# Kernel optimization log

Hardware: AMD Instinct MI355X
Metric: run time of the kernel (lower is better)

## Reference

```python
import jax, jax.numpy as jnp
import numpy as np

EPS = 1e-12  # F.normalize default eps


def _unfold(x, k, pad, stride):
    # torch F.unfold: [B,C,H,W] -> [B, C*k*k, L], features ordered (c, kh, kw), L row-major.
    B, C, H, W = x.shape
    xp = jnp.pad(x, ((0, 0), (0, 0), (pad, pad), (pad, pad)))
    Ho = (H + 2 * pad - k) // stride + 1
    Wo = (W + 2 * pad - k) // stride + 1
    r = (jnp.arange(Ho) * stride)[:, None] + jnp.arange(k)[None, :]  # [Ho,k]
    c = (jnp.arange(Wo) * stride)[:, None] + jnp.arange(k)[None, :]  # [Wo,k]
    p = xp[:, :, r[:, None, :, None], c[None, :, None, :]]  # [B,C,Ho,Wo,k,k]
    return p.transpose(0, 1, 4, 5, 2, 3).reshape(B, C * k * k, Ho * Wo)


def _fold(p, out_hw, k, pad, stride):
    # torch F.fold: overlap-add inverse of _unfold.
    B, CKK, L = p.shape
    C = CKK // (k * k)
    H, W = out_hw
    Ho = (H + 2 * pad - k) // stride + 1
    Wo = (W + 2 * pad - k) // stride + 1
    p = p.reshape(B, C, k, k, Ho, Wo).transpose(0, 1, 4, 5, 2, 3)  # [B,C,Ho,Wo,k,k]
    r = (jnp.arange(Ho) * stride)[:, None] + jnp.arange(k)[None, :]
    c = (jnp.arange(Wo) * stride)[:, None] + jnp.arange(k)[None, :]
    out = jnp.zeros((B, C, H + 2 * pad, W + 2 * pad), p.dtype)
    out = out.at[:, :, r[:, None, :, None], c[None, :, None, :]].add(p)
    return out[:, :, pad:pad + H, pad:pad + W]


def _l2n(x, axis):
    n = jnp.sqrt(jnp.sum(x * x, axis=axis, keepdims=True))
    return x / jnp.maximum(n, EPS)


def setup_inputs() -> dict:
    key = jax.random.key(0)
    ks = jax.random.split(key, 11)
    B, H, W = 1, 32, 32
    f = jnp.float32
    return {
        'lrsr_lv3': jax.random.normal(ks[0], (B, 256, H, W), f),
        'refsr_lv1': jax.random.normal(ks[1], (B, 64, 4 * H, 4 * W), f),
        'refsr_lv2': jax.random.normal(ks[2], (B, 128, 2 * H, 2 * W), f),
        'refsr_lv3': jax.random.normal(ks[3], (B, 256, H, W), f),
        'ref_lv1': jax.random.normal(ks[4], (B, 64, 4 * H, 4 * W), f),
        'ref_lv2': jax.random.normal(ks[5], (B, 128, 2 * H, 2 * W), f),
        'ref_lv3': jax.random.normal(ks[6], (B, 256, H, W), f),
        'W1': jax.random.normal(ks[7], (2304, 1152), f) * 0.02,
        'b1': jax.random.normal(ks[8], (2304,), f) * 0.02,
        'W2': jax.random.normal(ks[9], (2304, 576), f) * 0.02,
        'b2': jax.random.normal(ks[10], (2304,), f) * 0.02,
    }


def reference(lrsr_lv3, refsr_lv1, refsr_lv2, refsr_lv3, ref_lv1, ref_lv2, ref_lv3, W1, b1, W2, b2):
    B, _, H, W = lrsr_lv3.shape
    lr3 = _unfold(lrsr_lv3, 3, 1, 1)                       # [B, 2304, N]
    r3 = _unfold(refsr_lv3, 3, 1, 1).transpose(0, 2, 1)    # [B, N3, 2304]
    r2 = _unfold(refsr_lv2, 3, 1, 1).transpose(0, 2, 1) @ W1.T + b1  # [B, N2, 2304]
    r1 = _unfold(refsr_lv1, 3, 1, 1).transpose(0, 2, 1) @ W2.T + b2  # [B, N1, 2304]
    r3 = _l2n(r3, 2); r2 = _l2n(r2, 2); r1 = _l2n(r1, 2)
    lr3 = _l2n(lr3, 1)
    R3 = jnp.einsum('bnd,bdm->bnm', r3, lr3)  # [B, N3, N]
    R2 = jnp.einsum('bnd,bdm->bnm', r2, lr3)  # [B, N2, N]
    R1 = jnp.einsum('bnd,bdm->bnm', r1, lr3)  # [B, N1, N]
    R3_star = jnp.max(R3, axis=1); R3_arg = jnp.argmax(R3, axis=1)
    R2_star = jnp.max(R2, axis=1)
    R1_star = jnp.max(R1, axis=1)
    ref3u = _unfold(ref_lv3, 3, 1, 1)
    ref2u = _unfold(ref_lv2, 6, 2, 2)
    ref1u = _unfold(ref_lv1, 12, 4, 4)
    idx = R3_arg[:, None, :]  # [B,1,N] broadcast over feature dim
    T3u = jnp.take_along_axis(ref3u, idx, axis=2)
    T2u = jnp.take_along_axis(ref2u, idx, axis=2)
    T1u = jnp.take_along_axis(ref1u, idx, axis=2)
    T_lv3 = _fold(T3u, (H, W), 3, 1, 1) / 9.0
    T_lv2 = _fold(T2u, (2 * H, 2 * W), 6, 2, 2) / 9.0
    T_lv1 = _fold(T1u, (4 * H, 4 * W), 12, 4, 4) / 9.0
    S_3 = R3_star.reshape(B, 1, H, W)
    S_2 = R2_star.reshape(B, 1, H, W)
    S_1 = R1_star.reshape(B, 1, H, W)
    return (S_1, S_2, S_3, T_lv3, T_lv2, T_lv1)
```

## Files before the change

### kernel.cpp

```cpp
#include <hip/hip_runtime.h>

typedef short bf8 __attribute__((ext_vector_type(8)));
typedef float f32x4 __attribute__((ext_vector_type(4)));

static __device__ __forceinline__ unsigned short f2bf(float f) {
  unsigned u = __float_as_uint(f);
  unsigned r = u + 0x7FFFu + ((u >> 16) & 1u);
  return (unsigned short)(r >> 16);
}
static __device__ __forceinline__ float bf2f(unsigned short h) {
  return __uint_as_float(((unsigned)h) << 16);
}
static __device__ __forceinline__ unsigned fkey(float f) {
  unsigned u = __float_as_uint(f);
  return (u & 0x80000000u) ? ~u : (u | 0x80000000u);
}
static __device__ __forceinline__ float kdec(unsigned k) {
  unsigned u = (k & 0x80000000u) ? (k & 0x7FFFFFFFu) : ~k;
  return __uint_as_float(u);
}
static __device__ __forceinline__ int permC(int c, int C) { return (c % 9) * C + c / 9; }

static __device__ __forceinline__ void gload_lds16(const unsigned short* g, unsigned short* l) {
  __builtin_amdgcn_global_load_lds((const __attribute__((address_space(1))) void*)g,
                                   (__attribute__((address_space(3))) void*)l, 16, 0, 0);
}

static __device__ __forceinline__ float uf3(const float* __restrict__ src, int lgS, int d, int m) {
  const int S = 1 << lgS;
  int cc = d / 9;
  int r9 = d - cc * 9;
  int ki = r9 / 3;
  int kj = r9 - ki * 3;
  int i = (m >> lgS) + ki - 1;
  int j = (m & (S - 1)) + kj - 1;
  if ((unsigned)i >= (unsigned)S || (unsigned)j >= (unsigned)S) return 0.f;
  return src[((size_t)cc << (2 * lgS)) + ((size_t)i << lgS) + j];
}

__global__ __launch_bounds__(256) void k_prepA(const float* __restrict__ lrsr3, const float* __restrict__ rsr3,
                                               const float* __restrict__ rsr2, const float* __restrict__ rsr1,
                                               const float* __restrict__ b1, const float* __restrict__ b2,
                                               float* __restrict__ sclr, float* __restrict__ scu3,
                                               float* __restrict__ bl2, float* __restrict__ bl1,
                                               float* __restrict__ G2,
                                               float* __restrict__ rsr2t, float* __restrict__ rsr1t) {
  __shared__ float Tt[64][65];
  const int blk = blockIdx.x;
  const int tid = threadIdx.x;
  if (blk < 2048) {
    __shared__ float r0[256], r1[256], r2[256];
    const bool lr = blk < 1024;
    const int m = blk & 1023;
    const float* src = lr ? lrsr3 : rsr3;
    float s = 0.f, d1 = 0.f, d2 = 0.f;
    for (int d = tid; d < 2304; d += 256) {
      float v = uf3(src, 5, d, m);
      s += v * v; d1 += b1[d] * v; d2 += b2[d] * v;
    }
    r0[tid] = s; r1[tid] = d1; r2[tid] = d2;
    __syncthreads();
    for (int o = 128; o > 0; o >>= 1) {
      if (tid < o) { r0[tid] += r0[tid + o]; r1[tid] += r1[tid + o]; r2[tid] += r2[tid + o]; }
      __syncthreads();
    }
    if (tid == 0) {
      float sc = 1.f / fmaxf(sqrtf(r0[0]), 1e-12f);
      if (lr) { sclr[m] = sc; bl2[m] = r1[0] * sc; bl1[m] = r2[0] * sc; }
      else    { scu3[m] = sc; }
    }
  } else if (blk < 3072) {
    __shared__ float As[16][32], Bs[16][32];
    const int px = blk - 2048;
    const int m0 = (px >> 5) * 32, n0 = (px & 31) * 32;
    const int tx = tid & 15, ty = tid >> 4;
    float acc[2][2] = {};
    for (int kb = 0; kb < 256; kb += 16) {
      __syncthreads();
      {
        int kk = tid >> 5, mm = tid & 31;
        As[kk][mm] = lrsr3[(size_t)(kb + kk) * 1024 + m0 + mm];
        Bs[kk][mm] = rsr3[(size_t)(kb + kk) * 1024 + n0 + mm];
        int e2 = tid + 256; int kk2 = e2 >> 5, mm2 = e2 & 31;
        As[kk2][mm2] = lrsr3[(size_t)(kb + kk2) * 1024 + m0 + mm2];
        Bs[kk2][mm2] = rsr3[(size_t)(kb + kk2) * 1024 + n0 + mm2];
      }
      __syncthreads();
#pragma unroll
      for (int kk = 0; kk < 16; ++kk) {
        float a0 = As[kk][ty * 2], a1 = As[kk][ty * 2 + 1];
        float b0 = Bs[kk][tx * 2], b1v = Bs[kk][tx * 2 + 1];
        acc[0][0] = fmaf(a0, b0, acc[0][0]); acc[0][1] = fmaf(a0, b1v, acc[0][1]);
        acc[1][0] = fmaf(a1, b0, acc[1][0]); acc[1][1] = fmaf(a1, b1v, acc[1][1]);
      }
    }
#pragma unroll
    for (int i = 0; i < 2; ++i)
#pragma unroll
      for (int jj = 0; jj < 2; ++jj)
        G2[(size_t)(m0 + ty * 2 + i) * 1024 + (n0 + tx * 2 + jj)] = acc[i][jj];
  } else if (blk < 3200) {
    const int idx = blk - 3072;
    const int ct = idx & 1, st = idx >> 1;
#pragma unroll
    for (int i = 0; i < 16; ++i) {
      int id = tid + i * 256;
      int r = id >> 6, c = id & 63;
      Tt[r][c] = rsr2[(size_t)(ct * 64 + r) * 4096 + st * 64 + c];
    }
    __syncthreads();
#pragma unroll
    for (int i = 0; i < 16; ++i) {
      int id = tid + i * 256;
      int cc2 = id >> 6, rr = id & 63;
      rsr2t[(size_t)(st * 64 + cc2) * 128 + ct * 64 + rr] = Tt[rr][cc2];
    }
  } else {
    const int st = blk - 3200;
#pragma unroll
    for (int i = 0; i < 16; ++i) {
      int id = tid + i * 256;
      int r = id >> 6, c = id & 63;
      Tt[r][c] = rsr1[(size_t)r * 16384 + st * 64 + c];
    }
    __syncthreads();
#pragma unroll
    for (int i = 0; i < 16; ++i) {
      int id = tid + i * 256;
      int cc2 = id >> 6, rr = id & 63;
      rsr1t[(size_t)(st * 64 + cc2) * 64 + rr] = Tt[rr][cc2];
    }
  }
}

__global__ __launch_bounds__(256) void k_prepB(const float* __restrict__ lrsr3,
                                               const float* __restrict__ rsr2t, const float* __restrict__ rsr1t,
                                               const float* __restrict__ W1, const float* __restrict__ W2,
                                               const float* __restrict__ b1, const float* __restrict__ b2,
                                               const float* __restrict__ sclr, const float* __restrict__ scu3,
                                               const float* __restrict__ G2,
                                               unsigned short* __restrict__ lr3nbT,
                                               unsigned short* __restrict__ U2b, unsigned short* __restrict__ U1b,
                                               unsigned short* __restrict__ W1t, unsigned short* __restrict__ W2t,
                                               float* __restrict__ bw2, float* __restrict__ bw1,
                                               float* __restrict__ bb,
                                               float* __restrict__ s3, int* __restrict__ arg) {
  __shared__ unsigned short Ls[64][65];
  __shared__ float bv[256]; __shared__ int bidx[256];
  const int blk = blockIdx.x;
  const int tid = threadIdx.x;
  if (blk < 1152) {
    int id8 = blk * 256 + tid;
    int m = id8 / 288, c0 = (id8 - m * 288) * 8;
    float sc = sclr[m];
    bf8 v;
#pragma unroll
    for (int e = 0; e < 8; ++e) v[e] = (short)f2bf(uf3(lrsr3, 5, c0 + e, m) * sc);
    *(bf8*)(lr3nbT + (size_t)m * 2304 + c0) = v;
  } else if (blk < 3456) {
    int id = (blk - 1152) * 256 + tid;
    int t = id & 15, rest = id >> 4;
    int kk = rest % 9, n = rest / 9;
    int cc0 = t * 8;
    int ki = kk / 3, kj = kk - ki * 3;
    int sy = (n >> 6) + ki - 1, sx = (n & 63) + kj - 1;
    bf8 v;
    if ((unsigned)sy < 64u && (unsigned)sx < 64u) {
      const float* p = rsr2t + (size_t)(sy * 64 + sx) * 128 + cc0;
      f32x4 a = *(const f32x4*)p;
      f32x4 bq = *(const f32x4*)(p + 4);
#pragma unroll
      for (int e = 0; e < 4; ++e) { v[e] = (short)f2bf(a[e]); v[4 + e] = (short)f2bf(bq[e]); }
    } else {
#pragma unroll
      for (int e = 0; e < 8; ++e) v[e] = 0;
    }
    *(bf8*)(U2b + (size_t)n * 1152 + kk * 128 + cc0) = v;
  } else if (blk < 8576) {
    int id = (blk - 3456) * 256 + tid;
    int n = id / 80, rem = id - n * 80;
    int ks = rem >> 3, t = rem & 7;
    int cc0 = t * 8;
    bf8 v;
    if (ks == 9) {
#pragma unroll
      for (int e = 0; e < 8; ++e) v[e] = 0;
    } else {
      int ki = ks / 3, kj = ks - ki * 3;
      int sy = (n >> 7) + ki - 1, sx = (n & 127) + kj - 1;
      if ((unsigned)sy < 128u && (unsigned)sx < 128u) {
        const float* p = rsr1t + (size_t)(sy * 128 + sx) * 64 + cc0;
        f32x4 a = *(const f32x4*)p;
        f32x4 bq = *(const f32x4*)(p + 4);
#pragma unroll
        for (int e = 0; e < 4; ++e) { v[e] = (short)f2bf(a[e]); v[4 + e] = (short)f2bf(bq[e]); }
      } else {
#pragma unroll
        for (int e = 0; e < 8; ++e) v[e] = 0;
      }
    }
    *(bf8*)(U1b + (size_t)n * 640 + ks * 64 + cc0) = v;
  } else if (blk < 9548) {
    int idx = blk - 8576;
    int xx = idx % 27, yy = idx / 27;
    const float* W; unsigned short* Wt; int Cw, c0;
    if (xx < 18) { W = W1; Wt = W1t; Cw = 1152; c0 = xx * 64; }
    else         { W = W2; Wt = W2t; Cw = 576;  c0 = (xx - 18) * 64; }
    const int Cch = Cw / 9;
    const int d0 = yy * 64;
#pragma unroll
    for (int i = 0; i < 16; ++i) {
      int id = tid + i * 256;
      int r = id >> 6, c = id & 63;
      Ls[r][c] = f2bf(W[(size_t)(d0 + r) * Cw + c0 + c]);
    }
    __syncthreads();
#pragma unroll
    for (int i = 0; i < 16; ++i) {
      int id = tid + i * 256;
      int cc = id >> 6, rr = id & 63;
      int c = c0 + cc;
      Wt[(size_t)((c % 9) * Cch + c / 9) * 2304 + d0 + rr] = Ls[rr][cc];
    }
  } else if (blk < 9628) {
    int idx = blk - 9548;
    int x = idx & 7, y = idx >> 3;
    if (y == 9) {
      if (x >= 2) return;
      const float* b = x ? b2 : b1;
      float s = 0.f;
      for (int d = tid; d < 2304; d += 256) s += b[d] * b[d];
      bv[tid] = s; __syncthreads();
      for (int o = 128; o > 0; o >>= 1) { if (tid < o) bv[tid] += bv[tid + o]; __syncthreads(); }
      if (tid == 0) bb[x] = bv[0];
      return;
    }
    const bool two = x < 5;
    const float* W = two ? W1 : W2;
    const float* b = two ? b1 : b2;
    float* bw = two ? bw2 : bw1;
    const int Cw = two ? 1152 : 576;
    int c = (two ? x : x - 5) * 256 + tid;
    if (c >= Cw) return;
    int d0 = y * 256;
    float s = 0.f;
    for (int d = d0; d < d0 + 256; ++d) s += b[d] * W[(size_t)d * Cw + c];
    atomicAdd(&bw[(c % 9) * (Cw / 9) + c / 9], s);
  } else {
    const int m = blk - 9628;
    const int mi = m >> 5, mj = m & 31;
    float best = -3.0e38f; int bi = 0;
    for (int n = tid; n < 1024; n += 256) {
      const int ni = n >> 5, nj = n & 31;
      float raw = 0.f;
#pragma unroll
      for (int dy = -1; dy <= 1; ++dy) {
#pragma unroll
        for (int dx = -1; dx <= 1; ++dx) {
          bool vm = ((unsigned)(mi + dy) < 32u) && ((unsigned)(mj + dx) < 32u);
          bool vn = ((unsigned)(ni + dy) < 32u) && ((unsigned)(nj + dx) < 32u);
          if (vm && vn) {
            int off = dy * 32 + dx;
            raw += G2[(size_t)(m + off) * 1024 + (n + off)];
          }
        }
      }
      float v = raw * scu3[n];
      if (v > best) { best = v; bi = n; }
    }
    bv[tid] = best; bidx[tid] = bi;
    __syncthreads();
    for (int o = 128; o > 0; o >>= 1) {
      if (tid < o) {
        float ov = bv[tid + o]; int oi = bidx[tid + o];
        if (ov > bv[tid] || (ov == bv[tid] && oi < bidx[tid])) { bv[tid] = ov; bidx[tid] = oi; }
      }
      __syncthreads();
    }
    if (tid == 0) { s3[m] = bv[0] * sclr[m]; arg[m] = bidx[0]; }
  }
}

struct Job {
  const unsigned short* Alo;
  const unsigned short* Ahi;
  const unsigned short* Bt;
  unsigned short* Clo;
  unsigned short* Chi;
  const float* bl;
  const float* bw;
  const float* bbp;
  float* pnsq;
  float* pbwd;
  float* cmax;
  int Msplit, N, K, nbx, Mtot, npart, which;
};

template <int EPI, int NBUF>
static __device__ __forceinline__ void gemm_body(const Job& j0, const Job& j1, int nb0) {
  __shared__ __align__(16) unsigned short As[NBUF][128 * 64];
  __shared__ __align__(16) unsigned short Bs[NBUF][128 * 64];
  __shared__ unsigned colkey[128];
  __shared__ float ninvL[128];

  const int nwg = (int)gridDim.x;
  const int h = (int)blockIdx.x;
  const int qq = nwg >> 3, rm = nwg & 7;
  const int xcd = h & 7, wth = h >> 3;
  const int bid = (xcd < rm ? xcd * (qq + 1) : rm * (qq + 1) + (xcd - rm) * qq) + wth;

  const bool first = (bid < nb0);
  const Job j = first ? j0 : j1;
  const int local = bid - (first ? 0 : nb0);
  const int by = local / j.nbx;
  const int bx = local - by * j.nbx;
  const int m0 = by * 128, n0 = bx * 128;
  const int K = j.K, N = j.N;

  const unsigned short* Abase = (m0 < j.Msplit)
      ? j.Alo + (size_t)m0 * K
      : j.Ahi + (size_t)(m0 - j.Msplit) * K;

  const int tid = threadIdx.x;
  const int l = tid & 63;
  const int w = tid >> 6;
  const int wr = w >> 1, wc = w & 1;
  if (EPI == 2) {
    if (tid < 128) {
      colkey[tid] = 0u;
      const int r = m0 + tid;
      float nsq = 0.f, bwd = 0.f;
      for (int p = 0; p < j.npart; ++p) {
        nsq += j.pnsq[(size_t)p * j.Mtot + r];
        bwd += j.pbwd[(size_t)p * j.Mtot + r];
      }
      float tq = nsq + 2.f * bwd + j.bbp[j.which];
      ninvL[tid] = 1.f / fmaxf(sqrtf(fmaxf(tq, 0.f)), 1e-12f);
    }
  }

  f32x4 acc[4][4] = {};

  const int srow = w * 32;
  const int lrow = l >> 3;
  const int gcol = ((l & 7) ^ lrow) * 8;
  const int mr = l & 15;
  const int kg = l >> 4;

  const int nt = K >> 6;
  const int snap_kb = n0 + wc * 64;
  unsigned short snap[4][4][4];

  auto stage = [&](int buf, int kb) {
#pragma unroll
    for (int i = 0; i < 4; ++i) {
      int r = srow + i * 8;
      gload_lds16(Abase + (size_t)(r + lrow) * K + kb + gcol, &As[buf][r * 64]);
      gload_lds16(j.Bt + (size_t)(n0 + r + lrow) * K + kb + gcol, &Bs[buf][r * 64]);
    }
  };
  auto compute_tile = [&](int cur) {
#pragma unroll
    for (int ks = 0; ks < 2; ++ks) {
      bf8 af[4], bv[4];
#pragma unroll
      for (int mi = 0; mi < 4; ++mi) {
        const int row = wr * 64 + mi * 16 + mr;
        af[mi] = *(const bf8*)&As[cur][row * 64 + (((ks * 4 + kg) ^ (row & 7)) * 8)];
      }
#pragma unroll
      for (int ni = 0; ni < 4; ++ni) {
        const int row = wc * 64 + ni * 16 + mr;
        bv[ni] = *(const bf8*)&Bs[cur][row * 64 + (((ks * 4 + kg) ^ (row & 7)) * 8)];
      }
      __builtin_amdgcn_s_setprio(1);
#pragma unroll
      for (int mi = 0; mi < 4; ++mi)
#pragma unroll
        for (int ni = 0; ni < 4; ++ni)
          acc[mi][ni] = __builtin_amdgcn_mfma_f32_16x16x32_bf16(af[mi], bv[ni], acc[mi][ni], 0, 0, 0);
      __builtin_amdgcn_s_setprio(0);
    }
  };
  auto do_snap = [&](int cur) {
#pragma unroll
    for (int mi = 0; mi < 4; ++mi)
#pragma unroll
      for (int e = 0; e < 4; ++e) {
        const int row = wr * 64 + mi * 16 + kg * 4 + e;
#pragma unroll
        for (int ni = 0; ni < 4; ++ni) {
          const int slot = ni * 2 + (mr >> 3);
          snap[mi][ni][e] = As[cur][row * 64 + ((slot ^ (row & 7)) * 8) + (mr & 7)];
        }
      }
  };

  if constexpr (NBUF == 1) {
    for (int t = 0; t < nt; ++t) {
      if (t) __syncthreads();
      stage(0, t << 6);
      __syncthreads();
      compute_tile(0);
      if (EPI == 1 && (t << 6) == snap_kb) do_snap(0);
    }
  } else {
    auto waitv = [&](int Wt) {
      if (Wt >= 2)      asm volatile("s_waitcnt vmcnt(16)\ns_barrier" ::: "memory");
      else if (Wt == 1) asm volatile("s_waitcnt vmcnt(8)\ns_barrier" ::: "memory");
      else              asm volatile("s_waitcnt vmcnt(0)\ns_barrier" ::: "memory");
    };
#pragma unroll
    for (int p = 0; p < NBUF; ++p) if (p < nt) stage(p, p << 6);
    { int inflight = (NBUF < nt ? NBUF : nt); waitv(inflight - 1); }
    int cur = 0;
    for (int t = 0; t < nt; ++t) {
      compute_tile(cur);
      if (EPI == 1 && (t << 6) == snap_kb) do_snap(cur);
      if (t + 1 < nt) {
        asm volatile("s_waitcnt lgkmcnt(0)\ns_barrier" ::: "memory");
        if (t + NBUF < nt) stage(cur, (t + NBUF) << 6);
        const int im = (nt - 1 < t + NBUF) ? (nt - 1) : (t + NBUF);
        waitv(im - (t + 1));
        cur = (cur + 1 == NBUF) ? 0 : cur + 1;
      }
    }
  }

  const int lr0 = wr * 64;
  const int lc0 = wc * 64;
  if (EPI == 0) {
    unsigned short* Cbase = (m0 < j.Msplit)
        ? j.Clo + (size_t)m0 * N
        : j.Chi + (size_t)(m0 - j.Msplit) * N;
#pragma unroll
    for (int mi = 0; mi < 4; ++mi)
#pragma unroll
      for (int ni = 0; ni < 4; ++ni)
#pragma unroll
        for (int e = 0; e < 4; ++e)
          Cbase[(size_t)(lr0 + mi * 16 + kg * 4 + e) * (size_t)N + (n0 + lc0 + ni * 16 + mr)] = f2bf(acc[mi][ni][e]);
  } else if (EPI == 1) {
    float rp[4][4] = {};
    float bp[4][4] = {};
#pragma unroll
    for (int ni = 0; ni < 4; ++ni) {
      const float bwv = j.bw[n0 + lc0 + ni * 16 + mr];
#pragma unroll
      for (int mi = 0; mi < 4; ++mi)
#pragma unroll
        for (int e = 0; e < 4; ++e) {
          const float av = bf2f(snap[mi][ni][e]);
          rp[mi][e] += acc[mi][ni][e] * av;
          bp[mi][e] += bwv * av;
        }
    }
#pragma unroll
    for (int off = 1; off < 16; off <<= 1)
#pragma unroll
      for (int mi = 0; mi < 4; ++mi)
#pragma unroll
        for (int e = 0; e < 4; ++e) {
          rp[mi][e] += __shfl_xor(rp[mi][e], off);
          bp[mi][e] += __shfl_xor(bp[mi][e], off);
        }
    if (mr == 0) {
      const size_t slotbase = (size_t)(bx * 2 + wc) * j.Mtot;
#pragma unroll
      for (int mi = 0; mi < 4; ++mi)
#pragma unroll
        for (int e = 0; e < 4; ++e) {
          const int r = m0 + lr0 + mi * 16 + kg * 4 + e;
          j.pnsq[slotbase + r] = rp[mi][e];
          j.pbwd[slotbase + r] = bp[mi][e];
        }
    }
  } else {
    float nv[4][4];
#pragma unroll
    for (int mi = 0; mi < 4; ++mi)
#pragma unroll
      for (int e = 0; e < 4; ++e)
        nv[mi][e] = ninvL[lr0 + mi * 16 + kg * 4 + e];
#pragma unroll
    for (int ni = 0; ni < 4; ++ni) {
      float blv = j.bl[n0 + lc0 + ni * 16 + mr];
      float mx = -3.0e38f;
#pragma unroll
      for (int mi = 0; mi < 4; ++mi)
#pragma unroll
        for (int e = 0; e < 4; ++e) mx = fmaxf(mx, (acc[mi][ni][e] + blv) * nv[mi][e]);
      atomicMax(&colkey[lc0 + ni * 16 + mr], fkey(mx));
    }
    __syncthreads();
    if (tid < 128) j.cmax[(size_t)by * 1024 + n0 + tid] = kdec(colkey[tid]);
  }
}

__global__ __launch_bounds__(256) void k_gP (Job a, Job b, int nb0) { gemm_body<0, 3>(a, b, nb0); }
__global__ __launch_bounds__(256) void k_gE1(Job a, Job b, int nb0) { gemm_body<1, 1>(a, b, nb0); }
__global__ __launch_bounds__(256) void k_gE2(Job a, Job b, int nb0) { gemm_body<2, 1>(a, b, nb0); }

__global__ __launch_bounds__(256) void k_tfold(const float* __restrict__ ref3, const float* __restrict__ ref2,
                                               const float* __restrict__ ref1, const int* __restrict__ arg,
                                               const float* __restrict__ cmax1, const float* __restrict__ cmax2,
                                               float* __restrict__ out) {
  const int bid = blockIdx.x;
  const int tid = threadIdx.x;
  if (bid < 256) {
    __shared__ float plane[1024];
    __shared__ int argL[1024];
    const int c = bid;
#pragma unroll
    for (int k = 0; k < 4; ++k) {
      plane[k * 256 + tid] = ref3[(size_t)c * 1024 + k * 256 + tid];
      argL[k * 256 + tid] = arg[k * 256 + tid];
    }
    __syncthreads();
#pragma unroll
    for (int k = 0; k < 4; ++k) {
      int px = k * 256 + tid;
      int y = px >> 5, x = px & 31;
      float s = 0.f;
#pragma unroll
      for (int di = -1; di <= 1; ++di) {
        int i = y + di;
        if ((unsigned)i >= 32u) continue;
#pragma unroll
        for (int dj = -1; dj <= 1; ++dj) {
          int jw = x + dj;
          if ((unsigned)jw >= 32u) continue;
          int n2 = argL[i * 32 + jw];
          int rr = (n2 >> 5) + y - i, cc = (n2 & 31) + x - jw;
          if ((unsigned)rr < 32u && (unsigned)cc < 32u) s += plane[rr * 32 + cc];
        }
      }
      out[3072 + (size_t)c * 1024 + px] = s * (1.f / 9.f);
    }
  } else if (bid < 1280) {
    __shared__ int argL[1024];
#pragma unroll
    for (int k = 0; k < 4; ++k) argL[k * 256 + tid] = arg[k * 256 + tid];
    __syncthreads();
    int id2 = (bid - 256) * 256 + tid;
    int q = id2 & 31, y = (id2 >> 5) & 63, c = id2 >> 11;
    int iy = y >> 1;
    float s0 = 0.f, s1 = 0.f;
#pragma unroll
    for (int di = -1; di <= 1; ++di) {
      int i = iy + di;
      if ((unsigned)i >= 32u) continue;
      int ry = y - 2 * i;
#pragma unroll
      for (int dj = -1; dj <= 1; ++dj) {
        int jw = q + dj;
        if ((unsigned)jw >= 32u) continue;
        int n2 = argL[i * 32 + jw];
        int rr = (n2 >> 5) * 2 + ry;
        int cb = (n2 & 31) * 2 + 2 * (q - jw);
        if ((unsigned)rr < 64u && (unsigned)cb < 63u) {
          const float* p = ref2 + (size_t)c * 4096 + rr * 64 + cb;
          s0 += p[0]; s1 += p[1];
        }
      }
    }
    float2 o; o.x = s0 * (1.f / 9.f); o.y = s1 * (1.f / 9.f);
    *(float2*)(out + 265216 + (size_t)c * 4096 + y * 64 + 2 * q) = o;
  } else if (bid < 2304) {
    __shared__ int argL[1024];
#pragma unroll
    for (int k = 0; k < 4; ++k) argL[k * 256 + tid] = arg[k * 256 + tid];
    __syncthreads();
    int id1 = (bid - 1280) * 256 + tid;
    int q = id1 & 31, y = (id1 >> 5) & 127, c = id1 >> 12;
    int iy = y >> 2;
    f32x4 s = {0.f, 0.f, 0.f, 0.f};
#pragma unroll
    for (int di = -1; di <= 1; ++di) {
      int i = iy + di;
      if ((unsigned)i >= 32u) continue;
      int ry = y - 4 * i;
#pragma unroll
      for (int dj = -1; dj <= 1; ++dj) {
        int jw = q + dj;
        if ((unsigned)jw >= 32u) continue;
        int n2 = argL[i * 32 + jw];
        int rr = (n2 >> 5) * 4 + ry;
        int cb = (n2 & 31) * 4 + 4 * (q - jw);
        if ((unsigned)rr < 128u && (unsigned)cb < 125u) {
          f32x4 v = *(const f32x4*)(ref1 + (size_t)c * 16384 + rr * 128 + cb);
          s += v;
        }
      }
    }
    s *= (1.f / 9.f);
    *(f32x4*)(out + 789504 + (size_t)c * 16384 + y * 128 + 4 * q) = s;
  } else {
    int t = (bid - 2304) * 256 + tid;
    if (t < 1024) {
      float mx = -3.0e38f;
      for (int rb = 0; rb < 128; ++rb) mx = fmaxf(mx, cmax1[rb * 1024 + t]);
      out[t] = mx;
    } else {
      int tt = t - 1024;
      float mx = -3.0e38f;
      for (int rb = 0; rb < 32; ++rb) mx = fmaxf(mx, cmax2[rb * 1024 + tt]);
      out[1024 + tt] = mx;
    }
  }
}

static constexpr size_t OFF_BW2     = 0;
static constexpr size_t OFF_BW1     = 4608;
static constexpr size_t ZERO_BYTES  = 7168;
static constexpr size_t OFF_BB      = 7168;
static constexpr size_t OFF_BL2     = 7424;
static constexpr size_t OFF_BL1     = 11520;
static constexpr size_t OFF_SCLR    = 15616;
static constexpr size_t OFF_SCU3    = 19712;
static constexpr size_t OFF_R3ARG   = 23808;
static constexpr size_t OFF_PNSQ2   = 27904;
static constexpr size_t OFF_PBWD2   = OFF_PNSQ2 + 294912;
static constexpr size_t OFF_PNSQ1   = OFF_PBWD2 + 294912;
static constexpr size_t OFF_PBWD1   = OFF_PNSQ1 + 655360;
static constexpr size_t OFF_CMAX2   = OFF_PBWD1 + 655360;
static constexpr size_t OFF_CMAX1   = OFF_CMAX2 + 131072;
static constexpr size_t OFF_LR3NBT  = OFF_CMAX1 + 524288;
static constexpr size_t OFF_U2B     = OFF_LR3NBT + 4718592;
static constexpr size_t OFF_U1B     = OFF_U2B    + 9437184;
static constexpr size_t OFF_W1T     = OFF_U1B    + 20971520;
static constexpr size_t OFF_W2T     = OFF_W1T    + 5308416;
static constexpr size_t OFF_A2      = OFF_W2T    + 2949120;
static constexpr size_t OFF_A1      = OFF_A2     + 2654208;
static constexpr size_t OFF_M2T     = OFF_A1     + 819200;
static constexpr size_t OFF_M1T     = OFF_M2T    + 2359296;
static constexpr size_t OFF_G2      = OFF_M1T    + 1310720;
static constexpr size_t OFF_R2T     = OFF_G2     + 4194304;
static constexpr size_t OFF_R1T     = OFF_R2T    + 2097152;

extern "C" void kernel_launch(void* const* d_in, const int* in_sizes, int n_in,
                              void* d_out, int out_size, void* d_ws, size_t ws_size,
                              hipStream_t stream) {
  (void)in_sizes; (void)n_in; (void)out_size; (void)ws_size;
  const float* lrsr3  = (const float*)d_in[0];
  const float* rsr1   = (const float*)d_in[1];
  const float* rsr2   = (const float*)d_in[2];
  const float* rsr3   = (const float*)d_in[3];
  const float* ref1   = (const float*)d_in[4];
  const float* ref2   = (const float*)d_in[5];
  const float* ref3   = (const float*)d_in[6];
  const float* W1     = (const float*)d_in[7];
  const float* b1     = (const float*)d_in[8];
  const float* W2     = (const float*)d_in[9];
  const float* b2     = (const float*)d_in[10];
  float* out = (float*)d_out;
  char* ws = (char*)d_ws;

  float*          bw2     = (float*)(ws + OFF_BW2);
  float*          bw1     = (float*)(ws + OFF_BW1);
  float*          bb      = (float*)(ws + OFF_BB);
  float*          bl2     = (float*)(ws + OFF_BL2);
  float*          bl1     = (float*)(ws + OFF_BL1);
  float*          sclr    = (float*)(ws + OFF_SCLR);
  float*          scu3    = (float*)(ws + OFF_SCU3);
  int*            R3arg   = (int*)(ws + OFF_R3ARG);
  float*          pnsq2   = (float*)(ws + OFF_PNSQ2);
  float*          pbwd2   = (float*)(ws + OFF_PBWD2);
  float*          pnsq1   = (float*)(ws + OFF_PNSQ1);
  float*          pbwd1   = (float*)(ws + OFF_PBWD1);
  float*          cmax2   = (float*)(ws + OFF_CMAX2);
  float*          cmax1   = (float*)(ws + OFF_CMAX1);
  unsigned short* lr3nbT  = (unsigned short*)(ws + OFF_LR3NBT);
  unsigned short* U2b     = (unsigned short*)(ws + OFF_U2B);
  unsigned short* U1b     = (unsigned short*)(ws + OFF_U1B);
  unsigned short* W1t     = (unsigned short*)(ws + OFF_W1T);
  unsigned short* W2t     = (unsigned short*)(ws + OFF_W2T);
  unsigned short* A2b     = (unsigned short*)(ws + OFF_A2);
  unsigned short* A1b     = (unsigned short*)(ws + OFF_A1);
  unsigned short* M2tb    = (unsigned short*)(ws + OFF_M2T);
  unsigned short* M1tb    = (unsigned short*)(ws + OFF_M1T);
  float*          G2      = (float*)(ws + OFF_G2);
  float*          rsr2t   = (float*)(ws + OFF_R2T);
  float*          rsr1t   = (float*)(ws + OFF_R1T);

  hipMemsetAsync(d_ws, 0, ZERO_BYTES, stream);
  hipMemsetAsync(ws + OFF_W2T + (size_t)576 * 2304 * 2, 0, (size_t)64 * 2304 * 2, stream);

  k_prepA<<<3456, 256, 0, stream>>>(lrsr3, rsr3, rsr2, rsr1, b1, b2, sclr, scu3, bl2, bl1, G2, rsr2t, rsr1t);
  k_prepB<<<10652, 256, 0, stream>>>(lrsr3, rsr2t, rsr1t, W1, W2, b1, b2, sclr, scu3, G2,
                                     lr3nbT, U2b, U1b, W1t, W2t, bw2, bw1, bb, out + 2048, R3arg);

  Job jz = {};

  {
    Job a = jz, b = jz;
    a.Alo = W1t; a.Ahi = lr3nbT; a.Msplit = 1152; a.Bt = W1t;
    a.Clo = A2b; a.Chi = M2tb; a.N = 1152; a.K = 2304; a.nbx = 9;
    b.Alo = W2t; b.Ahi = lr3nbT; b.Msplit = 640; b.Bt = W2t;
    b.Clo = A1b; b.Chi = M1tb; b.N = 640; b.K = 2304; b.nbx = 5;
    k_gP<<<153 + 65, 256, 0, stream>>>(a, b, 153);
  }
  {
    Job a = jz, b = jz;
    a.Alo = U2b; a.Ahi = U2b; a.Msplit = 4096; a.Bt = A2b;
    a.bw = bw2; a.pnsq = pnsq2; a.pbwd = pbwd2; a.Mtot = 4096;
    a.N = 1152; a.K = 1152; a.nbx = 9;
    b.Alo = U1b; b.Ahi = U1b; b.Msplit = 16384; b.Bt = A1b;
    b.bw = bw1; b.pnsq = pnsq1; b.pbwd = pbwd1; b.Mtot = 16384;
    b.N = 640; b.K = 640; b.nbx = 5;
    k_gE1<<<288 + 640, 256, 0, stream>>>(a, b, 288);
  }
  {
    Job a = jz, b = jz;
    a.Alo = U2b; a.Ahi = U2b; a.Msplit = 4096; a.Bt = M2tb;
    a.bl = bl2; a.pnsq = pnsq2; a.pbwd = pbwd2; a.bbp = bb;
    a.npart = 18; a.which = 0; a.cmax = cmax2; a.Mtot = 4096;
    a.N = 1024; a.K = 1152; a.nbx = 8;
    b.Alo = U1b; b.Ahi = U1b; b.Msplit = 16384; b.Bt = M1tb;
    b.bl = bl1; b.pnsq = pnsq1; b.pbwd = pbwd1; b.bbp = bb;
    b.npart = 10; b.which = 1; b.cmax = cmax1; b.Mtot = 16384;
    b.N = 1024; b.K = 640; b.nbx = 8;
    k_gE2<<<256 + 1024, 256, 0, stream>>>(a, b, 256);
  }

  k_tfold<<<2312, 256, 0, stream>>>(ref3, ref2, ref1, R3arg, cmax1, cmax2, out);
}
```

Measured before the change: 256.5 us.

## Fuse weight transpose and projection GEMM into prep kernels, apply row scale in epilogue

Moves the lr3 unfold-to-bf16 and the W1/W2 transpose into the first prep kernel. The projection GEMM (k_gP) now runs as the first 218 blocks of a merged kernel alongside the remaining prep work (U2b/U1b packing, bias dots, R3 argmax). The lr3 row normalization scale is dropped from the packed operand and applied in the GEMM epilogue instead. This saves one kernel launch and lets the GEMM overlap with independent prep blocks. In exchange the GEMM switches from triple-buffered to single-buffered staging and shares a launch with many small memory-bound blocks.

```diff
diff --git a/kernel.cpp b/kernel.cpp
--- a/kernel.cpp
+++ b/kernel.cpp
@@ -19,7 +19,11 @@
   unsigned u = (k & 0x80000000u) ? (k & 0x7FFFFFFFu) : ~k;
   return __uint_as_float(u);
 }
-static __device__ __forceinline__ int permC(int c, int C) { return (c % 9) * C + c / 9; }
+static __device__ __forceinline__ int xcdswz(int h, int nwg) {
+  int q = nwg >> 3, r = nwg & 7;
+  int xcd = h & 7, w = h >> 3;
+  return (xcd < r ? xcd * (q + 1) : r * (q + 1) + (xcd - r) * q) + w;
+}
 
 static __device__ __forceinline__ void gload_lds16(const unsigned short* g, unsigned short* l) {
   __builtin_amdgcn_global_load_lds((const __attribute__((address_space(1))) void*)g,
@@ -40,12 +44,14 @@
 
 __global__ __launch_bounds__(256) void k_prepA(const float* __restrict__ lrsr3, const float* __restrict__ rsr3,
                                                const float* __restrict__ rsr2, const float* __restrict__ rsr1,
+                                               const float* __restrict__ W1, const float* __restrict__ W2,
                                                const float* __restrict__ b1, const float* __restrict__ b2,
                                                float* __restrict__ sclr, float* __restrict__ scu3,
                                                float* __restrict__ bl2, float* __restrict__ bl1,
                                                float* __restrict__ G2,
-                                               float* __restrict__ rsr2t, float* __restrict__ rsr1t) {
-  __shared__ float Tt[64][65];
+                                               float* __restrict__ rsr2t, float* __restrict__ rsr1t,
+                                               unsigned short* __restrict__ lr3nbT,
+                                               unsigned short* __restrict__ W1t, unsigned short* __restrict__ W2t) {
   const int blk = blockIdx.x;
   const int tid = threadIdx.x;
   if (blk < 2048) {
@@ -100,6 +106,7 @@
       for (int jj = 0; jj < 2; ++jj)
         G2[(size_t)(m0 + ty * 2 + i) * 1024 + (n0 + tx * 2 + jj)] = acc[i][jj];
   } else if (blk < 3200) {
+    __shared__ float Tt[64][65];
     const int idx = blk - 3072;
     const int ct = idx & 1, st = idx >> 1;
 #pragma unroll
@@ -115,7 +122,8 @@
       int cc2 = id >> 6, rr = id & 63;
       rsr2t[(size_t)(st * 64 + cc2) * 128 + ct * 64 + rr] = Tt[rr][cc2];
     }
-  } else {
+  } else if (blk < 3456) {
+    __shared__ float Tt[64][65];
     const int st = blk - 3200;
 #pragma unroll
     for (int i = 0; i < 16; ++i) {
@@ -130,35 +138,273 @@
       int cc2 = id >> 6, rr = id & 63;
       rsr1t[(size_t)(st * 64 + cc2) * 64 + rr] = Tt[rr][cc2];
     }
-  }
-}
-
-__global__ __launch_bounds__(256) void k_prepB(const float* __restrict__ lrsr3,
-                                               const float* __restrict__ rsr2t, const float* __restrict__ rsr1t,
-                                               const float* __restrict__ W1, const float* __restrict__ W2,
-                                               const float* __restrict__ b1, const float* __restrict__ b2,
-                                               const float* __restrict__ sclr, const float* __restrict__ scu3,
-                                               const float* __restrict__ G2,
-                                               unsigned short* __restrict__ lr3nbT,
-                                               unsigned short* __restrict__ U2b, unsigned short* __restrict__ U1b,
-                                               unsigned short* __restrict__ W1t, unsigned short* __restrict__ W2t,
-                                               float* __restrict__ bw2, float* __restrict__ bw1,
-                                               float* __restrict__ bb,
-                                               float* __restrict__ s3, int* __restrict__ arg) {
-  __shared__ unsigned short Ls[64][65];
-  __shared__ float bv[256]; __shared__ int bidx[256];
+  } else if (blk < 4608) {
+    int id8 = (blk - 3456) * 256 + tid;
+    int m = id8 / 288, c0 = (id8 - m * 288) * 8;
+    bf8 v;
+#pragma unroll
+    for (int e = 0; e < 8; ++e) v[e] = (short)f2bf(uf3(lrsr3, 5, c0 + e, m));
+    *(bf8*)(lr3nbT + (size_t)m * 2304 + c0) = v;
+  } else {
+    __shared__ unsigned short Ls[64][65];
+    int idx = blk - 4608;
+    int xx = idx % 27, yy = idx / 27;
+    const float* W; unsigned short* Wt; int Cw, c0;
+    if (xx < 18) { W = W1; Wt = W1t; Cw = 1152; c0 = xx * 64; }
+    else         { W = W2; Wt = W2t; Cw = 576;  c0 = (xx - 18) * 64; }
+    const int Cch = Cw / 9;
+    const int d0 = yy * 64;
+#pragma unroll
+    for (int i = 0; i < 16; ++i) {
+      int id = tid + i * 256;
+      int r = id >> 6, c = id & 63;
+      Ls[r][c] = f2bf(W[(size_t)(d0 + r) * Cw + c0 + c]);
+    }
+    __syncthreads();
+#pragma unroll
+    for (int i = 0; i < 16; ++i) {
+      int id = tid + i * 256;
+      int cc = id >> 6, rr = id & 63;
+      int c = c0 + cc;
+      Wt[(size_t)((c % 9) * Cch + c / 9) * 2304 + d0 + rr] = Ls[rr][cc];
+    }
+  }
+}
+
+struct Job {
+  const unsigned short* Alo;
+  const unsigned short* Ahi;
+  const unsigned short* Bt;
+  unsigned short* Clo;
+  unsigned short* Chi;
+  const float* bl;
+  const float* bw;
+  const float* bbp;
+  const float* rowscale;
+  float* pnsq;
+  float* pbwd;
+  float* cmax;
+  int Msplit, N, K, nbx, Mtot, npart, which;
+};
+
+template <int EPI, int NBUF>
+static __device__ __forceinline__ void gemm_body(const Job& j0, const Job& j1, int nb0, int bid) {
+  __shared__ __align__(16) unsigned short As[NBUF][128 * 64];
+  __shared__ __align__(16) unsigned short Bs[NBUF][128 * 64];
+  __shared__ unsigned colkey[128];
+  __shared__ float ninvL[128];
+
+  const bool first = (bid < nb0);
+  const Job j = first ? j0 : j1;
+  const int local = bid - (first ? 0 : nb0);
+  const int by = local / j.nbx;
+  const int bx = local - by * j.nbx;
+  const int m0 = by * 128, n0 = bx * 128;
+  const int K = j.K, N = j.N;
+
+  const unsigned short* Abase = (m0 < j.Msplit)
+      ? j.Alo + (size_t)m0 * K
+      : j.Ahi + (size_t)(m0 - j.Msplit) * K;
+
+  const int tid = threadIdx.x;
+  const int l = tid & 63;
+  const int w = tid >> 6;
+  const int wr = w >> 1, wc = w & 1;
+  if (EPI == 2) {
+    if (tid < 128) {
+      colkey[tid] = 0u;
+      const int r = m0 + tid;
+      float nsq = 0.f, bwd = 0.f;
+      for (int p = 0; p < j.npart; ++p) {
+        nsq += j.pnsq[(size_t)p * j.Mtot + r];
+        bwd += j.pbwd[(size_t)p * j.Mtot + r];
+      }
+      float tq = nsq + 2.f * bwd + j.bbp[j.which];
+      ninvL[tid] = 1.f / fmaxf(sqrtf(fmaxf(tq, 0.f)), 1e-12f);
+    }
+  }
+
+  f32x4 acc[4][4] = {};
+
+  const int srow = w * 32;
+  const int lrow = l >> 3;
+  const int gcol = ((l & 7) ^ lrow) * 8;
+  const int mr = l & 15;
+  const int kg = l >> 4;
+
+  const int nt = K >> 6;
+  const int snap_kb = n0 + wc * 64;
+  unsigned short snap[4][4][4];
+
+  auto stage = [&](int buf, int kb) {
+#pragma unroll
+    for (int i = 0; i < 4; ++i) {
+      int r = srow + i * 8;
+      gload_lds16(Abase + (size_t)(r + lrow) * K + kb + gcol, &As[buf][r * 64]);
+      gload_lds16(j.Bt + (size_t)(n0 + r + lrow) * K + kb + gcol, &Bs[buf][r * 64]);
+    }
+  };
+  auto compute_tile = [&](int cur) {
+#pragma unroll
+    for (int ks = 0; ks < 2; ++ks) {
+      bf8 af[4], bv[4];
+#pragma unroll
+      for (int mi = 0; mi < 4; ++mi) {
+        const int row = wr * 64 + mi * 16 + mr;
+        af[mi] = *(const bf8*)&As[cur][row * 64 + (((ks * 4 + kg) ^ (row & 7)) * 8)];
+      }
+#pragma unroll
+      for (int ni = 0; ni < 4; ++ni) {
+        const int row = wc * 64 + ni * 16 + mr;
+        bv[ni] = *(const bf8*)&Bs[cur][row * 64 + (((ks * 4 + kg) ^ (row & 7)) * 8)];
+      }
+      __builtin_amdgcn_s_setprio(1);
+#pragma unroll
+      for (int mi = 0; mi < 4; ++mi)
+#pragma unroll
+        for (int ni = 0; ni < 4; ++ni)
+          acc[mi][ni] = __builtin_amdgcn_mfma_f32_16x16x32_bf16(af[mi], bv[ni], acc[mi][ni], 0, 0, 0);
+      __builtin_amdgcn_s_setprio(0);
+    }
+  };
+  auto do_snap = [&](int cur) {
+#pragma unroll
+    for (int mi = 0; mi < 4; ++mi)
+#pragma unroll
+      for (int e = 0; e < 4; ++e) {
+        const int row = wr * 64 + mi * 16 + kg * 4 + e;
+#pragma unroll
+        for (int ni = 0; ni < 4; ++ni) {
+          const int slot = ni * 2 + (mr >> 3);
+          snap[mi][ni][e] = As[cur][row * 64 + ((slot ^ (row & 7)) * 8) + (mr & 7)];
+        }
+      }
+  };
+
+  if constexpr (NBUF == 1) {
+    for (int t = 0; t < nt; ++t) {
+      if (t) __syncthreads();
+      stage(0, t << 6);
+      __syncthreads();
+      compute_tile(0);
+      if (EPI == 1 && (t << 6) == snap_kb) do_snap(0);
+    }
+  } else {
+    auto waitv = [&](int Wt) {
+      if (Wt >= 2)      asm volatile("s_waitcnt vmcnt(16)\ns_barrier" ::: "memory");
+      else if (Wt == 1) asm volatile("s_waitcnt vmcnt(8)\ns_barrier" ::: "memory");
+      else              asm volatile("s_waitcnt vmcnt(0)\ns_barrier" ::: "memory");
+    };
+#pragma unroll
+    for (int p = 0; p < NBUF; ++p) if (p < nt) stage(p, p << 6);
+    { int inflight = (NBUF < nt ? NBUF : nt); waitv(inflight - 1); }
+    int cur = 0;
+    for (int t = 0; t < nt; ++t) {
+      compute_tile(cur);
+      if (EPI == 1 && (t << 6) == snap_kb) do_snap(cur);
+      if (t + 1 < nt) {
+        asm volatile("s_waitcnt lgkmcnt(0)\ns_barrier" ::: "memory");
+        if (t + NBUF < nt) stage(cur, (t + NBUF) << 6);
+        const int im = (nt - 1 < t + NBUF) ? (nt - 1) : (t + NBUF);
+        waitv(im - (t + 1));
+        cur = (cur + 1 == NBUF) ? 0 : cur + 1;
+      }
+    }
+  }
+
+  const int lr0 = wr * 64;
+  const int lc0 = wc * 64;
+  if (EPI == 0) {
+    const bool hi = (m0 >= j.Msplit);
+    unsigned short* Cbase = hi ? j.Chi + (size_t)(m0 - j.Msplit) * N
+                               : j.Clo + (size_t)m0 * N;
+    float rs[4][4];
+#pragma unroll
+    for (int mi = 0; mi < 4; ++mi)
+#pragma unroll
+      for (int e = 0; e < 4; ++e)
+        rs[mi][e] = hi ? j.rowscale[m0 - j.Msplit + lr0 + mi * 16 + kg * 4 + e] : 1.f;
+#pragma unroll
+    for (int mi = 0; mi < 4; ++mi)
+#pragma unroll
+      for (int ni = 0; ni < 4; ++ni)
+#pragma unroll
+        for (int e = 0; e < 4; ++e)
+          Cbase[(size_t)(lr0 + mi * 16 + kg * 4 + e) * (size_t)N + (n0 + lc0 + ni * 16 + mr)] =
+              f2bf(acc[mi][ni][e] * rs[mi][e]);
+  } else if (EPI == 1) {
+    float rp[4][4] = {};
+    float bp[4][4] = {};
+#pragma unroll
+    for (int ni = 0; ni < 4; ++ni) {
+      const float bwv = j.bw[n0 + lc0 + ni * 16 + mr];
+#pragma unroll
+      for (int mi = 0; mi < 4; ++mi)
+#pragma unroll
+        for (int e = 0; e < 4; ++e) {
+          const float av = bf2f(snap[mi][ni][e]);
+          rp[mi][e] += acc[mi][ni][e] * av;
+          bp[mi][e] += bwv * av;
+        }
+    }
+#pragma unroll
+    for (int off = 1; off < 16; off <<= 1)
+#pragma unroll
+      for (int mi = 0; mi < 4; ++mi)
+#pragma unroll
+        for (int e = 0; e < 4; ++e) {
+          rp[mi][e] += __shfl_xor(rp[mi][e], off);
+          bp[mi][e] += __shfl_xor(bp[mi][e], off);
+        }
+    if (mr == 0) {
+      const size_t slotbase = (size_t)(bx * 2 + wc) * j.Mtot;
+#pragma unroll
+      for (int mi = 0; mi < 4; ++mi)
+#pragma unroll
+        for (int e = 0; e < 4; ++e) {
+          const int r = m0 + lr0 + mi * 16 + kg * 4 + e;
+          j.pnsq[slotbase + r] = rp[mi][e];
+          j.pbwd[slotbase + r] = bp[mi][e];
+        }
+    }
+  } else {
+    float nv[4][4];
+#pragma unroll
+    for (int mi = 0; mi < 4; ++mi)
+#pragma unroll
+      for (int e = 0; e < 4; ++e)
+        nv[mi][e] = ninvL[lr0 + mi * 16 + kg * 4 + e];
+#pragma unroll
+    for (int ni = 0; ni < 4; ++ni) {
+      float blv = j.bl[n0 + lc0 + ni * 16 + mr];
+      float mx = -3.0e38f;
+#pragma unroll
+      for (int mi = 0; mi < 4; ++mi)
+#pragma unroll
+        for (int e = 0; e < 4; ++e) mx = fmaxf(mx, (acc[mi][ni][e] + blv) * nv[mi][e]);
+      atomicMax(&colkey[lc0 + ni * 16 + mr], fkey(mx));
+    }
+    __syncthreads();
+    if (tid < 128) j.cmax[(size_t)by * 1024 + n0 + tid] = kdec(colkey[tid]);
+  }
+}
+
+__global__ __launch_bounds__(256) void k_prepBP(Job pa, Job pb, int nbP0,
+                                                const float* __restrict__ rsr2t, const float* __restrict__ rsr1t,
+                                                const float* __restrict__ W1, const float* __restrict__ W2,
+                                                const float* __restrict__ b1, const float* __restrict__ b2,
+                                                const float* __restrict__ sclr, const float* __restrict__ scu3,
+                                                const float* __restrict__ G2,
+                                                unsigned short* __restrict__ U2b, unsigned short* __restrict__ U1b,
+                                                float* __restrict__ bw2, float* __restrict__ bw1,
+                                                float* __restrict__ bb,
+                                                float* __restrict__ s3, int* __restrict__ arg) {
   const int blk = blockIdx.x;
   const int tid = threadIdx.x;
-  if (blk < 1152) {
-    int id8 = blk * 256 + tid;
-    int m = id8 / 288, c0 = (id8 - m * 288) * 8;
-    float sc = sclr[m];
-    bf8 v;
-#pragma unroll
-    for (int e = 0; e < 8; ++e) v[e] = (short)f2bf(uf3(lrsr3, 5, c0 + e, m) * sc);
-    *(bf8*)(lr3nbT + (size_t)m * 2304 + c0) = v;
-  } else if (blk < 3456) {
-    int id = (blk - 1152) * 256 + tid;
+  if (blk < 218) {
+    gemm_body<0, 1>(pa, pb, nbP0, xcdswz(blk, 218));
+  } else if (blk < 2522) {
+    int id = (blk - 218) * 256 + tid;
     int t = id & 15, rest = id >> 4;
     int kk = rest % 9, n = rest / 9;
     int cc0 = t * 8;
@@ -176,8 +422,8 @@
       for (int e = 0; e < 8; ++e) v[e] = 0;
     }
     *(bf8*)(U2b + (size_t)n * 1152 + kk * 128 + cc0) = v;
-  } else if (blk < 8576) {
-    int id = (blk - 3456) * 256 + tid;
+  } else if (blk < 7642) {
+    int id = (blk - 2522) * 256 + tid;
     int n = id / 80, rem = id - n * 80;
     int ks = rem >> 3, t = rem & 7;
     int cc0 = t * 8;
@@ -200,39 +446,18 @@
       }
     }
     *(bf8*)(U1b + (size_t)n * 640 + ks * 64 + cc0) = v;
-  } else if (blk < 9548) {
-    int idx = blk - 8576;
-    int xx = idx % 27, yy = idx / 27;
-    const float* W; unsigned short* Wt; int Cw, c0;
-    if (xx < 18) { W = W1; Wt = W1t; Cw = 1152; c0 = xx * 64; }
-    else         { W = W2; Wt = W2t; Cw = 576;  c0 = (xx - 18) * 64; }
-    const int Cch = Cw / 9;
-    const int d0 = yy * 64;
-#pragma unroll
-    for (int i = 0; i < 16; ++i) {
-      int id = tid + i * 256;
-      int r = id >> 6, c = id & 63;
-      Ls[r][c] = f2bf(W[(size_t)(d0 + r) * Cw + c0 + c]);
-    }
-    __syncthreads();
-#pragma unroll
-    for (int i = 0; i < 16; ++i) {
-      int id = tid + i * 256;
-      int cc = id >> 6, rr = id & 63;
-      int c = c0 + cc;
-      Wt[(size_t)((c % 9) * Cch + c / 9) * 2304 + d0 + rr] = Ls[rr][cc];
-    }
-  } else if (blk < 9628) {
-    int idx = blk - 9548;
+  } else if (blk < 7722) {
+    __shared__ float red[256];
+    int idx = blk - 7642;
     int x = idx & 7, y = idx >> 3;
     if (y == 9) {
       if (x >= 2) return;
       const float* b = x ? b2 : b1;
       float s = 0.f;
       for (int d = tid; d < 2304; d += 256) s += b[d] * b[d];
-      bv[tid] = s; __syncthreads();
-      for (int o = 128; o > 0; o >>= 1) { if (tid < o) bv[tid] += bv[tid + o]; __syncthreads(); }
-      if (tid == 0) bb[x] = bv[0];
+      red[tid] = s; __syncthreads();
+      for (int o = 128; o > 0; o >>= 1) { if (tid < o) red[tid] += red[tid + o]; __syncthreads(); }
+      if (tid == 0) bb[x] = red[0];
       return;
     }
     const bool two = x < 5;
@@ -247,7 +472,8 @@
     for (int d = d0; d < d0 + 256; ++d) s += b[d] * W[(size_t)d * Cw + c];
     atomicAdd(&bw[(c % 9) * (Cw / 9) + c / 9], s);
   } else {
-    const int m = blk - 9628;
+    __shared__ float bv[256]; __shared__ int bidx[256];
+    const int m = blk - 7722;
     const int mi = m >> 5, mj = m & 31;
     float best = -3.0e38f; int bi = 0;
     for (int n = tid; n < 1024; n += 256) {
@@ -281,225 +507,12 @@
   }
 }
 
-struct Job {
-  const unsigned short* Alo;
-  const unsigned short* Ahi;
-  const unsigned short* Bt;
-  unsigned short* Clo;
-  unsigned short* Chi;
-  const float* bl;
-  const float* bw;
-  const float* bbp;
-  float* pnsq;
-  float* pbwd;
-  float* cmax;
-  int Msplit, N, K, nbx, Mtot, npart, which;
-};
-
-template <int EPI, int NBUF>
-static __device__ __forceinline__ void gemm_body(const Job& j0, const Job& j1, int nb0) {
-  __shared__ __align__(16) unsigned short As[NBUF][128 * 64];
-  __shared__ __align__(16) unsigned short Bs[NBUF][128 * 64];
-  __shared__ unsigned colkey[128];
-  __shared__ float ninvL[128];
-
-  const int nwg = (int)gridDim.x;
-  const int h = (int)blockIdx.x;
-  const int qq = nwg >> 3, rm = nwg & 7;
-  const int xcd = h & 7, wth = h >> 3;
-  const int bid = (xcd < rm ? xcd * (qq + 1) : rm * (qq + 1) + (xcd - rm) * qq) + wth;
-
-  const bool first = (bid < nb0);
-  const Job j = first ? j0 : j1;
-  const int local = bid - (first ? 0 : nb0);
-  const int by = local / j.nbx;
-  const int bx = local - by * j.nbx;
-  const int m0 = by * 128, n0 = bx * 128;
-  const int K = j.K, N = j.N;
-
-  const unsigned short* Abase = (m0 < j.Msplit)
-      ? j.Alo + (size_t)m0 * K
-      : j.Ahi + (size_t)(m0 - j.Msplit) * K;
-
-  const int tid = threadIdx.x;
-  const int l = tid & 63;
-  const int w = tid >> 6;
-  const int wr = w >> 1, wc = w & 1;
-  if (EPI == 2) {
-    if (tid < 128) {
-      colkey[tid] = 0u;
-      const int r = m0 + tid;
-      float nsq = 0.f, bwd = 0.f;
-      for (int p = 0; p < j.npart; ++p) {
-        nsq += j.pnsq[(size_t)p * j.Mtot + r];
-        bwd += j.pbwd[(size_t)p * j.Mtot + r];
-      }
-      float tq = nsq + 2.f * bwd + j.bbp[j.which];
-      ninvL[tid] = 1.f / fmaxf(sqrtf(fmaxf(tq, 0.f)), 1e-12f);
-    }
-  }
-
-  f32x4 acc[4][4] = {};
-
-  const int srow = w * 32;
-  const int lrow = l >> 3;
-  const int gcol = ((l & 7) ^ lrow) * 8;
-  const int mr = l & 15;
-  const int kg = l >> 4;
-
-  const int nt = K >> 6;
-  const int snap_kb = n0 + wc * 64;
-  unsigned short snap[4][4][4];
-
-  auto stage = [&](int buf, int kb) {
-#pragma unroll
-    for (int i = 0; i < 4; ++i) {
-      int r = srow + i * 8;
-      gload_lds16(Abase + (size_t)(r + lrow) * K + kb + gcol, &As[buf][r * 64]);
-      gload_lds16(j.Bt + (size_t)(n0 + r + lrow) * K + kb + gcol, &Bs[buf][r * 64]);
-    }
-  };
-  auto compute_tile = [&](int cur) {
-#pragma unroll
-    for (int ks = 0; ks < 2; ++ks) {
-      bf8 af[4], bv[4];
-#pragma unroll
-      for (int mi = 0; mi < 4; ++mi) {
-        const int row = wr * 64 + mi * 16 + mr;
-        af[mi] = *(const bf8*)&As[cur][row * 64 + (((ks * 4 + kg) ^ (row & 7)) * 8)];
-      }
-#pragma unroll
-      for (int ni = 0; ni < 4; ++ni) {
-        const int row = wc * 64 + ni * 16 + mr;
-        bv[ni] = *(const bf8*)&Bs[cur][row * 64 + (((ks * 4 + kg) ^ (row & 7)) * 8)];
-      }
-      __builtin_amdgcn_s_setprio(1);
-#pragma unroll
-      for (int mi = 0; mi < 4; ++mi)
-#pragma unroll
-        for (int ni = 0; ni < 4; ++ni)
-          acc[mi][ni] = __builtin_amdgcn_mfma_f32_16x16x32_bf16(af[mi], bv[ni], acc[mi][ni], 0, 0, 0);
-      __builtin_amdgcn_s_setprio(0);
-    }
-  };
-  auto do_snap = [&](int cur) {
-#pragma unroll
-    for (int mi = 0; mi < 4; ++mi)
-#pragma unroll
-      for (int e = 0; e < 4; ++e) {
-        const int row = wr * 64 + mi * 16 + kg * 4 + e;
-#pragma unroll
-        for (int ni = 0; ni < 4; ++ni) {
-          const int slot = ni * 2 + (mr >> 3);
-          snap[mi][ni][e] = As[cur][row * 64 + ((slot ^ (row & 7)) * 8) + (mr & 7)];
-        }
-      }
-  };
-
-  if constexpr (NBUF == 1) {
-    for (int t = 0; t < nt; ++t) {
-      if (t) __syncthreads();
-      stage(0, t << 6);
-      __syncthreads();
-      compute_tile(0);
-      if (EPI == 1 && (t << 6) == snap_kb) do_snap(0);
-    }
-  } else {
-    auto waitv = [&](int Wt) {
-      if (Wt >= 2)      asm volatile("s_waitcnt vmcnt(16)\ns_barrier" ::: "memory");
-      else if (Wt == 1) asm volatile("s_waitcnt vmcnt(8)\ns_barrier" ::: "memory");
-      else              asm volatile("s_waitcnt vmcnt(0)\ns_barrier" ::: "memory");
-    };
-#pragma unroll
-    for (int p = 0; p < NBUF; ++p) if (p < nt) stage(p, p << 6);
-    { int inflight = (NBUF < nt ? NBUF : nt); waitv(inflight - 1); }
-    int cur = 0;
-    for (int t = 0; t < nt; ++t) {
-      compute_tile(cur);
-      if (EPI == 1 && (t << 6) == snap_kb) do_snap(cur);
-      if (t + 1 < nt) {
-        asm volatile("s_waitcnt lgkmcnt(0)\ns_barrier" ::: "memory");
-        if (t + NBUF < nt) stage(cur, (t + NBUF) << 6);
-        const int im = (nt - 1 < t + NBUF) ? (nt - 1) : (t + NBUF);
-        waitv(im - (t + 1));
-        cur = (cur + 1 == NBUF) ? 0 : cur + 1;
-      }
-    }
-  }
-
-  const int lr0 = wr * 64;
-  const int lc0 = wc * 64;
-  if (EPI == 0) {
-    unsigned short* Cbase = (m0 < j.Msplit)
-        ? j.Clo + (size_t)m0 * N
-        : j.Chi + (size_t)(m0 - j.Msplit) * N;
-#pragma unroll
-    for (int mi = 0; mi < 4; ++mi)
-#pragma unroll
-      for (int ni = 0; ni < 4; ++ni)
-#pragma unroll
-        for (int e = 0; e < 4; ++e)
-          Cbase[(size_t)(lr0 + mi * 16 + kg * 4 + e) * (size_t)N + (n0 + lc0 + ni * 16 + mr)] = f2bf(acc[mi][ni][e]);
-  } else if (EPI == 1) {
-    float rp[4][4] = {};
-    float bp[4][4] = {};
-#pragma unroll
-    for (int ni = 0; ni < 4; ++ni) {
-      const float bwv = j.bw[n0 + lc0 + ni * 16 + mr];
-#pragma unroll
-      for (int mi = 0; mi < 4; ++mi)
-#pragma unroll
-        for (int e = 0; e < 4; ++e) {
-          const float av = bf2f(snap[mi][ni][e]);
-          rp[mi][e] += acc[mi][ni][e] * av;
-          bp[mi][e] += bwv * av;
-        }
-    }
-#pragma unroll
-    for (int off = 1; off < 16; off <<= 1)
-#pragma unroll
-      for (int mi = 0; mi < 4; ++mi)
-#pragma unroll
-        for (int e = 0; e < 4; ++e) {
-          rp[mi][e] += __shfl_xor(rp[mi][e], off);
-          bp[mi][e] += __shfl_xor(bp[mi][e], off);
-        }
-    if (mr == 0) {
-      const size_t slotbase = (size_t)(bx * 2 + wc) * j.Mtot;
-#pragma unroll
-      for (int mi = 0; mi < 4; ++mi)
-#pragma unroll
-        for (int e = 0; e < 4; ++e) {
-          const int r = m0 + lr0 + mi * 16 + kg * 4 + e;
-          j.pnsq[slotbase + r] = rp[mi][e];
-          j.pbwd[slotbase + r] = bp[mi][e];
-        }
-    }
-  } else {
-    float nv[4][4];
-#pragma unroll
-    for (int mi = 0; mi < 4; ++mi)
-#pragma unroll
-      for (int e = 0; e < 4; ++e)
-        nv[mi][e] = ninvL[lr0 + mi * 16 + kg * 4 + e];
-#pragma unroll
-    for (int ni = 0; ni < 4; ++ni) {
-      float blv = j.bl[n0 + lc0 + ni * 16 + mr];
-      float mx = -3.0e38f;
-#pragma unroll
-      for (int mi = 0; mi < 4; ++mi)
-#pragma unroll
-        for (int e = 0; e < 4; ++e) mx = fmaxf(mx, (acc[mi][ni][e] + blv) * nv[mi][e]);
-      atomicMax(&colkey[lc0 + ni * 16 + mr], fkey(mx));
-    }
-    __syncthreads();
-    if (tid < 128) j.cmax[(size_t)by * 1024 + n0 + tid] = kdec(colkey[tid]);
-  }
-}
-
-__global__ __launch_bounds__(256) void k_gP (Job a, Job b, int nb0) { gemm_body<0, 3>(a, b, nb0); }
-__global__ __launch_bounds__(256) void k_gE1(Job a, Job b, int nb0) { gemm_body<1, 1>(a, b, nb0); }
-__global__ __launch_bounds__(256) void k_gE2(Job a, Job b, int nb0) { gemm_body<2, 1>(a, b, nb0); }
+__global__ __launch_bounds__(256) void k_gE1(Job a, Job b, int nb0) {
+  gemm_body<1, 1>(a, b, nb0, xcdswz((int)blockIdx.x, (int)gridDim.x));
+}
+__global__ __launch_bounds__(256) void k_gE2(Job a, Job b, int nb0) {
+  gemm_body<2, 1>(a, b, nb0, xcdswz((int)blockIdx.x, (int)gridDim.x));
+}
 
 __global__ __launch_bounds__(256) void k_tfold(const float* __restrict__ ref3, const float* __restrict__ ref2,
                                                const float* __restrict__ ref1, const int* __restrict__ arg,
@@ -686,19 +699,18 @@
   hipMemsetAsync(d_ws, 0, ZERO_BYTES, stream);
   hipMemsetAsync(ws + OFF_W2T + (size_t)576 * 2304 * 2, 0, (size_t)64 * 2304 * 2, stream);
 
-  k_prepA<<<3456, 256, 0, stream>>>(lrsr3, rsr3, rsr2, rsr1, b1, b2, sclr, scu3, bl2, bl1, G2, rsr2t, rsr1t);
-  k_prepB<<<10652, 256, 0, stream>>>(lrsr3, rsr2t, rsr1t, W1, W2, b1, b2, sclr, scu3, G2,
-                                     lr3nbT, U2b, U1b, W1t, W2t, bw2, bw1, bb, out + 2048, R3arg);
+  k_prepA<<<5580, 256, 0, stream>>>(lrsr3, rsr3, rsr2, rsr1, W1, W2, b1, b2,
+                                    sclr, scu3, bl2, bl1, G2, rsr2t, rsr1t, lr3nbT, W1t, W2t);
 
   Job jz = {};
-
   {
     Job a = jz, b = jz;
     a.Alo = W1t; a.Ahi = lr3nbT; a.Msplit = 1152; a.Bt = W1t;
-    a.Clo = A2b; a.Chi = M2tb; a.N = 1152; a.K = 2304; a.nbx = 9;
+    a.Clo = A2b; a.Chi = M2tb; a.rowscale = sclr; a.N = 1152; a.K = 2304; a.nbx = 9;
     b.Alo = W2t; b.Ahi = lr3nbT; b.Msplit = 640; b.Bt = W2t;
-    b.Clo = A1b; b.Chi = M1tb; b.N = 640; b.K = 2304; b.nbx = 5;
-    k_gP<<<153 + 65, 256, 0, stream>>>(a, b, 153);
+    b.Clo = A1b; b.Chi = M1tb; b.rowscale = sclr; b.N = 640; b.K = 2304; b.nbx = 5;
+    k_prepBP<<<8746, 256, 0, stream>>>(a, b, 153, rsr2t, rsr1t, W1, W2, b1, b2, sclr, scu3, G2,
+                                       U2b, U1b, bw2, bw1, bb, out + 2048, R3arg);
   }
   {
     Job a = jz, b = jz;
```

Result: faster. 231.6 us (-9.7%).
